# Kernel tuning notes

Measured on AMD Instinct MI355X. Metric: run time of the kernel, lower is better.

Reference implementation:

```python
import jax, jax.numpy as jnp
import numpy as np

N = 100000   # nodes
E = 1600000  # edges
IN = 3       # in_channels
H = 32       # hidden_channels
C = 10       # num_classes_dynamic (== num output classes here)
G = 64       # number of graphs in the batch


def setup_inputs() -> dict:
    key = jax.random.key(0)
    ks = jax.random.split(key, 12)
    def w(k, shape, fan_in):
        return jax.random.normal(k, shape, jnp.float32) / np.sqrt(fan_in).astype(np.float32)
    inp = {}
    inp["x"] = jax.random.normal(ks[0], (N, IN), jnp.float32)
    inp["edge_index"] = jax.random.randint(ks[1], (2, E), 0, N, jnp.int32)
    inp["batch"] = jnp.sort(jax.random.randint(ks[2], (N,), 0, G, jnp.int32))
    # per-class linear filters (DynamicEdgeConv.filters)
    inp["filt_W"] = w(ks[3], (C, IN, H), IN)
    inp["filt_b"] = jnp.zeros((C, H), jnp.float32)
    # shared edge MLP: Linear(2H,H) -> ReLU -> Linear(H,H)
    inp["mlp_W1"] = w(ks[4], (2 * H, H), 2 * H)
    inp["mlp_b1"] = jnp.zeros((H,), jnp.float32)
    inp["mlp_W2"] = w(ks[5], (H, H), H)
    inp["mlp_b2"] = jnp.zeros((H,), jnp.float32)
    # GCN layers (gcn1 input dim hardcoded 323 = IN + C*H)
    inp["gcn1_W"] = w(ks[6], (IN + C * H, H), IN + C * H)
    inp["gcn1_b"] = jnp.zeros((H,), jnp.float32)
    inp["gcn2_W"] = w(ks[7], (H, H), H)
    inp["gcn2_b"] = jnp.zeros((H,), jnp.float32)
    # classifier
    inp["cls_W"] = w(ks[8], (H, C), H)
    inp["cls_b"] = jnp.zeros((C,), jnp.float32)
    return inp


def _gcn_conv(x, W, b, row, col, dinv):
    # PyG GCNConv: add self-loops, sym-normalize, aggregate src->dst
    xw = x @ W                                   # [N, H]
    norm = dinv[row] * dinv[col]                 # [E]
    out = jax.ops.segment_sum(xw[row] * norm[:, None], col, num_segments=x.shape[0])
    out = out + xw * (dinv * dinv)[:, None]      # self-loop term, norm = 1/deg_i
    return out + b


def _forward(x, edge_index, batch, filt_W, filt_b, mlp_W1, mlp_b1, mlp_W2, mlp_b2,
             gcn1_W, gcn1_b, gcn2_W, gcn2_b, cls_W, cls_b):
    row, col = edge_index[0], edge_index[1]
    n = x.shape[0]

    # DynamicEdgeConv: per-class filter -> gather(row,col) -> edge MLP -> scatter_add into col
    def per_class(_, wb):
        Wc, bc = wb
        xc = x @ Wc + bc                                      # [N, H]
        ef = jnp.concatenate([xc[row], xc[col]], axis=1)      # [E, 2H]
        h = jax.nn.relu(ef @ mlp_W1 + mlp_b1) @ mlp_W2 + mlp_b2
        return None, jax.ops.segment_sum(h, col, num_segments=n)
    _, aggs = jax.lax.scan(per_class, None, (filt_W, filt_b))  # [C, N, H]

    feat = jnp.concatenate([x, aggs.transpose(1, 0, 2).reshape(n, -1)], axis=1)  # [N, IN + C*H]

    deg = jax.ops.segment_sum(jnp.ones(row.shape[0], x.dtype), col, num_segments=n) + 1.0
    dinv = deg ** -0.5
    h1 = jax.nn.relu(_gcn_conv(feat, gcn1_W, gcn1_b, row, col, dinv))
    h2 = jax.nn.relu(_gcn_conv(h1, gcn2_W, gcn2_b, row, col, dinv))

    counts = jax.ops.segment_sum(jnp.ones(n, x.dtype), batch, num_segments=G)
    pooled = jax.ops.segment_sum(h2, batch, num_segments=G) / jnp.maximum(counts, 1.0)[:, None]
    return pooled @ cls_W + cls_b                             # [G, C]


def reference(x, edge_index, batch, filt_W, filt_b, mlp_W1, mlp_b1, mlp_W2, mlp_b2,
              gcn1_W, gcn1_b, gcn2_W, gcn2_b, cls_W, cls_b):
    return _forward(x, edge_index, batch, filt_W, filt_b, mlp_W1, mlp_b1, mlp_W2, mlp_b2,
                    gcn1_W, gcn1_b, gcn2_W, gcn2_b, cls_W, cls_b)
```

## Files before the change

### kernel.cpp

```cpp
#include <hip/hip_runtime.h>

#define NN 100000
#define NE 1600000
#define HH 32
#define CC 10
#define GG 64
#define NB 391
#define PBLK 100
#define ECH 16000
#define MTOT (NB * PBLK)
#define MSB ((MTOT + 255) / 256)

typedef _Float16 half8 __attribute__((ext_vector_type(8)));
typedef _Float16 half2v __attribute__((ext_vector_type(2)));
typedef float f32x4 __attribute__((ext_vector_type(4)));

__device__ __forceinline__ half2v bch(int v) { return __builtin_bit_cast(half2v, v); }


__global__ void precompute_small(const float* __restrict__ fW, const float* __restrict__ fb,
                                 const float* __restrict__ W1, const float* __restrict__ b1,
                                 const float* __restrict__ W2, const float* __restrict__ b2,
                                 const float* __restrict__ g1W, float* __restrict__ tab,
                                 _Float16* __restrict__ Mfrag) {
    int c = blockIdx.x;
    int k = threadIdx.x >> 5;
    int j = threadIdx.x & 31;
    float m = 0.f;
    for (int mm = 0; mm < 32; ++mm)
        m += W2[k * 32 + mm] * g1W[(3 + 32 * c + mm) * 32 + j];
    tab[2240 + c * 1024 + k * 32 + j] = m;

    if (k < 3) {
        float a = 0.f, b = 0.f;
        for (int i = 0; i < 32; ++i) {
            float w = fW[c * 96 + k * 32 + i];
            a += w * W1[i * 32 + j];
            b += w * W1[(32 + i) * 32 + j];
        }
        tab[c * 96 + k * 32 + j] = a;
        tab[960 + c * 96 + k * 32 + j] = b;
    } else if (k == 3) {
        float h = b1[j];
        for (int i = 0; i < 32; ++i)
            h += fb[c * 32 + i] * (W1[i * 32 + j] + W1[(32 + i) * 32 + j]);
        tab[1920 + c * 32 + j] = h;
    } else if (k == 4 && c == 0) {
        float t = 0.f;
        for (int cc2 = 0; cc2 < CC; ++cc2)
            for (int mm = 0; mm < 32; ++mm)
                t += b2[mm] * g1W[(3 + 32 * cc2 + mm) * 32 + j];
        tab[12480 + j] = t;
    }
    __syncthreads();
    {
        int jch = k;
        int jcol = j;
        float v = tab[2240 + c * 1024 + jch * 32 + jcol];
        int knew = (c >> 1) * 64 + 2 * jch + (c & 1);
        int kc = knew >> 5, within = knew & 31;
        int jt = jcol >> 4;
        int lq = within >> 3, ii = within & 7;
        int lidx = lq * 16 + (jcol & 15);
        int flat = ((kc * 2 + jt) * 64 + lidx) * 8 + ii;
        Mfrag[flat] = (_Float16)v;
    }
}

__global__ void bucket_hist(const int* __restrict__ ei, int* __restrict__ mat) {
    __shared__ int h[NB];
    int blk = blockIdx.x, tid = threadIdx.x;
    for (int i = tid; i < NB; i += 256) h[i] = 0;
    __syncthreads();
    int base = blk * ECH;
    for (int k = tid; k < ECH; k += 256)
        atomicAdd(&h[ei[NE + base + k] >> 8], 1);
    __syncthreads();
    for (int i = tid; i < NB; i += 256) mat[i * PBLK + blk] = h[i];
}

__global__ void scan_m1(const int* __restrict__ mat, int* __restrict__ msum) {
    __shared__ int sh[256];
    int b = blockIdx.x, t = threadIdx.x;
    int i = b * 256 + t;
    sh[t] = (i < MTOT) ? mat[i] : 0;
    __syncthreads();
    for (int off = 128; off > 0; off >>= 1) {
        if (t < off) sh[t] += sh[t + off];
        __syncthreads();
    }
    if (t == 0) msum[b] = sh[0];
}

__global__ void scan_m2(int* __restrict__ msum, float* __restrict__ pooled) {
    for (int i = threadIdx.x; i < GG * 33; i += 256) pooled[i] = 0.0f;
    __shared__ int sh[256];
    int t = threadIdx.x;
    int v = (t < MSB) ? msum[t] : 0;
    sh[t] = v;
    __syncthreads();
    for (int off = 1; off < 256; off <<= 1) {
        int add = (t >= off) ? sh[t - off] : 0;
        __syncthreads();
        sh[t] += add;
        __syncthreads();
    }
    if (t < MSB) msum[t] = sh[t] - v;
}

__global__ void scan_m3(int* __restrict__ mat, const int* __restrict__ msum) {
    __shared__ int sh[256];
    int b = blockIdx.x, t = threadIdx.x;
    int i = b * 256 + t;
    int v = (i < MTOT) ? mat[i] : 0;
    sh[t] = v;
    __syncthreads();
    for (int off = 1; off < 256; off <<= 1) {
        int add = (t >= off) ? sh[t - off] : 0;
        __syncthreads();
        sh[t] += add;
        __syncthreads();
    }
    if (i < MTOT) mat[i] = sh[t] - v + msum[b];
}

__global__ void bucket_scatter(const int* __restrict__ ei, const int* __restrict__ mat,
                               unsigned int* __restrict__ part) {
    __shared__ int bas[NB];
    __shared__ int cur[NB];
    int blk = blockIdx.x, tid = threadIdx.x;
    for (int i = tid; i < NB; i += 256) { bas[i] = mat[i * PBLK + blk]; cur[i] = 0; }
    __syncthreads();
    int base = blk * ECH;
    for (int k = tid; k < ECH; k += 256) {
        int e = base + k;
        int r = ei[e];
        int c = ei[NE + e];
        int b = c >> 8;
        int local = atomicAdd(&cur[b], 1);
        part[bas[b] + local] = (unsigned)r | ((unsigned)(c & 255) << 24);
    }
}

__global__ void bucket_build(const unsigned int* __restrict__ part, const int* __restrict__ mat,
                             const float* __restrict__ x, int* __restrict__ csr_row,
                             int* __restrict__ ideg, int* __restrict__ offs,
                             float* __restrict__ dinv, float4* __restrict__ xpad,
                             uint4* __restrict__ xs) {
    __shared__ int lh[256];
    __shared__ int lex[256];
    __shared__ int cur[256];
    int b = blockIdx.x, tid = threadIdx.x;
    int ebase = mat[b * PBLK];
    int eend = (b == NB - 1) ? NE : mat[(b + 1) * PBLK];
    int m = eend - ebase;
    lh[tid] = 0;
    __syncthreads();
    for (int k = tid; k < m; k += 256) {
        unsigned v = part[ebase + k];
        atomicAdd(&lh[v >> 24], 1);
    }
    __syncthreads();
    int cnt = lh[tid];
    lex[tid] = cnt;
    __syncthreads();
    for (int off = 1; off < 256; off <<= 1) {
        int v = (tid >= off) ? lex[tid - off] : 0;
        __syncthreads();
        lex[tid] += v;
        __syncthreads();
    }
    int excl = lex[tid] - cnt;
    lex[tid] = excl;
    cur[tid] = 0;
    int n = b * 256 + tid;
    if (n < NN) {
        ideg[n] = cnt;
        offs[n] = ebase + excl;
        float di = rsqrtf((float)cnt + 1.0f);
        dinv[n] = di;
        float x0 = x[n * 3], x1 = x[n * 3 + 1], x2 = x[n * 3 + 2];
        xpad[n] = make_float4(x0, x1, x2, di);
        _Float16 hx = (_Float16)x0, hy = (_Float16)x1, hz = (_Float16)x2;
        half2v sx = {hx, hx}, sy = {hy, hy}, sz = {hz, hz};
        xs[n] = make_uint4(__builtin_bit_cast(unsigned int, sx),
                           __builtin_bit_cast(unsigned int, sy),
                           __builtin_bit_cast(unsigned int, sz), 0u);
    }
    if (b == 0 && tid == 0) offs[NN] = NE;
    __syncthreads();
    for (int k = tid; k < m; k += 256) {
        unsigned v = part[ebase + k];
        int cl = (int)(v >> 24);
        int r = (int)(v & 0x00FFFFFFu);
        int local = atomicAdd(&cur[cl], 1);
        csr_row[ebase + lex[cl] + local] = r;
    }
}

#define EC_PAIR(QQ, SRC) do { \
    half2v px_ = bch(__shfl((int)(QQ).x, (SRC), 64)); \
    half2v py_ = bch(__shfl((int)(QQ).y, (SRC), 64)); \
    half2v pz_ = bch(__shfl((int)(QQ).z, (SRC), 64)); \
    _Pragma("unroll") \
    for (int p = 0; p < 5; ++p) { \
        half2v v = va[p] + px_ * A0[p] + py_ * A1[p] + pz_ * A2[p]; \
        v = __builtin_elementwise_max(v, zero); \
        acc[p] += v; \
    } } while (0)

#define EC_FLUSH() do { \
    _Pragma("unroll") \
    for (int p = 0; p < 5; ++p) { \
        accf[2 * p]     += (float)acc[p].x; \
        accf[2 * p + 1] += (float)acc[p].y; \
        acc[p] = zero; \
    } } while (0)

#define EC_CHUNK_FROM(T0, QQ, C2) do { \
    int tfull_ = (C2) >> 1; \
    int t_ = (T0); \
    for (; t_ + 4 <= tfull_; t_ += 4) { \
        _Pragma("unroll") \
        for (int u = 0; u < 4; ++u) EC_PAIR(QQ, 2 * (t_ + u) + half); \
        EC_FLUSH(); \
    } \
    for (; t_ < tfull_; ++t_) EC_PAIR(QQ, 2 * t_ + half); \
    if ((C2) & 1) { \
        int src_ = (C2) - 1; \
        half2v px_ = bch(__shfl((int)(QQ).x, src_, 64)); \
        half2v py_ = bch(__shfl((int)(QQ).y, src_, 64)); \
        half2v pz_ = bch(__shfl((int)(QQ).z, src_, 64)); \
        if (half == 0) { \
            _Pragma("unroll") \
            for (int p = 0; p < 5; ++p) { \
                half2v v = va[p] + px_ * A0[p] + py_ * A1[p] + pz_ * A2[p]; \
                v = __builtin_elementwise_max(v, zero); \
                acc[p] += v; \
            } \
        } \
    } \
    EC_FLUSH(); } while (0)

__global__ __launch_bounds__(256, 4) void edgeconv_fused(
    const uint4* __restrict__ xs, const int* __restrict__ offs,
    const int* __restrict__ csr_row, const float* __restrict__ tab,
    _Float16* __restrict__ aggh) {
    int lane = threadIdx.x & 63;
    int j = lane & 31;
    int half = lane >> 5;

    half2v A0[5], A1[5], A2[5], B0[5], B1[5], B2[5], hb[5];
#pragma unroll
    for (int p = 0; p < 5; ++p) {
        int c0 = 2 * p, c1 = 2 * p + 1;
        A0[p] = half2v{(_Float16)tab[c0 * 96 + j],        (_Float16)tab[c1 * 96 + j]};
        A1[p] = half2v{(_Float16)tab[c0 * 96 + 32 + j],   (_Float16)tab[c1 * 96 + 32 + j]};
        A2[p] = half2v{(_Float16)tab[c0 * 96 + 64 + j],   (_Float16)tab[c1 * 96 + 64 + j]};
        B0[p] = half2v{(_Float16)tab[960 + c0 * 96 + j],      (_Float16)tab[960 + c1 * 96 + j]};
        B1[p] = half2v{(_Float16)tab[960 + c0 * 96 + 32 + j], (_Float16)tab[960 + c1 * 96 + 32 + j]};
        B2[p] = half2v{(_Float16)tab[960 + c0 * 96 + 64 + j], (_Float16)tab[960 + c1 * 96 + 64 + j]};
        hb[p] = half2v{(_Float16)tab[1920 + c0 * 32 + j], (_Float16)tab[1920 + c1 * 32 + j]};
    }
    const half2v zero = half2v{(_Float16)0.f, (_Float16)0.f};

    int wid = blockIdx.x * 4 + (threadIdx.x >> 6);
    const int ws = gridDim.x * 4;

    int n = wid;
    if (n >= NN) return;
    int e0 = offs[n];
    int e1 = offs[n + 1];
    uint4 qn = xs[n];
    int n2 = n + ws;
    int e0n = 0, e1n = 0;
    if (n2 < NN) { e0n = offs[n2]; e1n = offs[n2 + 1]; }
    uint4 q;
    {
        int ee = e0 + lane;
        int r0 = (ee < e1) ? csr_row[ee] : 0;
        q = xs[r0];
    }

    while (true) {
        int n3 = n2 + ws;
        int e0n2 = 0, e1n2 = 0;
        if (n3 < NN) { e0n2 = offs[n3]; e1n2 = offs[n3 + 1]; }
        uint4 qn2 = make_uint4(0u, 0u, 0u, 0u);
        if (n2 < NN) qn2 = xs[n2];

        bool multi = (e1 - e0) > 64;
        int pb = multi ? (e0 + 64) : e0n;
        int pe = multi ? e1 : e1n;
        int ee2 = pb + lane;
        int rn = (ee2 < pe) ? csr_row[ee2] : 0;

        half2v pxn = bch((int)qn.x), pyn = bch((int)qn.y), pzn = bch((int)qn.z);
        half2v va[5], acc[5];
        float accf[10];
#pragma unroll
        for (int p = 0; p < 5; ++p) {
            va[p] = hb[p] + pxn * B0[p] + pyn * B1[p] + pzn * B2[p];
            acc[p] = zero;
            accf[2 * p] = 0.f;
            accf[2 * p + 1] = 0.f;
        }

        int c2 = e1 - e0;
        if (c2 > 64) c2 = 64;
        int t0 = 0;
        if ((c2 >> 1) >= 4) {
#pragma unroll
            for (int u = 0; u < 4; ++u) EC_PAIR(q, 2 * u + half);
            EC_FLUSH();
            t0 = 4;
        }
        uint4 qpre = xs[rn];
        EC_CHUNK_FROM(t0, q, c2);

        if (multi) {
            int base = e0 + 64;
            uint4 qc = qpre;
            while (true) {
                int cc = e1 - base;
                if (cc > 64) cc = 64;
                int nb = base + 64;
                bool m2 = nb < e1;
                int pb2 = m2 ? nb : e0n;
                int pe2 = m2 ? e1 : e1n;
                int ee3 = pb2 + lane;
                int rn2 = (ee3 < pe2) ? csr_row[ee3] : 0;
                uint4 qp2 = xs[rn2];
                EC_CHUNK_FROM(0, qc, cc);
                qc = qp2;
                if (!m2) break;
                base = nb;
            }
            qpre = qc;
        }

#pragma unroll
        for (int c = 0; c < 10; ++c) accf[c] += __shfl_xor(accf[c], 32, 64);
        unsigned* arow32 = (unsigned*)(aggh + (size_t)n * 320);
        half2v d0 = {(_Float16)accf[2 * half],     (_Float16)accf[2 * half + 1]};
        half2v d1 = {(_Float16)accf[4 + 2 * half], (_Float16)accf[4 + 2 * half + 1]};
        arow32[lane]      = __builtin_bit_cast(unsigned, d0);
        arow32[64 + lane] = __builtin_bit_cast(unsigned, d1);
        if (half == 0) {
            half2v d2 = {(_Float16)accf[8], (_Float16)accf[9]};
            arow32[128 + lane] = __builtin_bit_cast(unsigned, d2);
        }

        if (n2 >= NN) return;
        n = n2;
        n2 = n3;
        e0 = e0n; e1 = e1n;
        e0n = e0n2; e1n = e1n2;
        qn = qn2;
        q = qpre;
    }
}

__global__ __launch_bounds__(256) void fold_mfma(
    const _Float16* __restrict__ aggh, const _Float16* __restrict__ MfragG,
    const float4* __restrict__ xpad, const int* __restrict__ ideg,
    const float* __restrict__ tab, const float* __restrict__ g1W,
    _Float16* __restrict__ y1) {
    __shared__ _Float16 Mf[10240];
    {
        const uint4* src = (const uint4*)MfragG;
        uint4* dst = (uint4*)Mf;
        for (int i = threadIdx.x; i < 1280; i += 256) dst[i] = src[i];
    }
    __syncthreads();

    int wave = blockIdx.x * 4 + (threadIdx.x >> 6);
    int lane = threadIdx.x & 63;
    int n0 = wave * 16;
    if (n0 >= NN) return;

    int m = lane & 15, q = lane >> 4;
    int arow_n = n0 + m;
    bool rowok = arow_n < NN;
    const _Float16* arow = aggh + (size_t)arow_n * 320 + q * 8;

    const half8* mf = (const half8*)Mf;
    f32x4 acc0 = {0.f, 0.f, 0.f, 0.f};
    f32x4 acc1 = {0.f, 0.f, 0.f, 0.f};

    for (int kc = 0; kc < 10; ++kc) {
        half8 a;
        if (rowok) a = *(const half8*)(arow + kc * 32);
        else {
#pragma unroll
            for (int i = 0; i < 8; ++i) a[i] = (_Float16)0.f;
        }
        half8 b0 = mf[(kc * 2 + 0) * 64 + lane];
        half8 b1 = mf[(kc * 2 + 1) * 64 + lane];
        acc0 = __builtin_amdgcn_mfma_f32_16x16x32_f16(a, b0, acc0, 0, 0, 0);
        acc1 = __builtin_amdgcn_mfma_f32_16x16x32_f16(a, b1, acc1, 0, 0, 0);
    }

    int jcol = lane & 15;
    float t0 = tab[12480 + jcol],      t1 = tab[12480 + 16 + jcol];
    float w00 = g1W[jcol],      w01 = g1W[32 + jcol],      w02 = g1W[64 + jcol];
    float w10 = g1W[16 + jcol], w11 = g1W[48 + jcol],      w12 = g1W[80 + jcol];
#pragma unroll
    for (int r = 0; r < 4; ++r) {
        int node = n0 + q * 4 + r;
        if (node < NN) {
            float4 xn = xpad[node];
            float dg = (float)ideg[node];
            float v0 = dg * t0 + xn.x * w00 + xn.y * w01 + xn.z * w02 + acc0[r];
            float v1 = dg * t1 + xn.x * w10 + xn.y * w11 + xn.z * w12 + acc1[r];
            y1[node * 32 + jcol]      = (_Float16)(v0 * xn.w);
            y1[node * 32 + 16 + jcol] = (_Float16)(v1 * xn.w);
        }
    }
}

__global__ __launch_bounds__(256, 8) void prop1_fused(
    const int* __restrict__ offs, const int* __restrict__ csr_row,
    const unsigned int* __restrict__ y1p, const float* __restrict__ dinv,
    const float* __restrict__ g1b, const float* __restrict__ g2W,
    unsigned int* __restrict__ y2p) {
    __shared__ float g2s[1024];
    for (int i = threadIdx.x; i < 1024; i += 256) g2s[i] = g2W[i];
    __syncthreads();

    int lane = threadIdx.x & 63;
    int l = lane & 15;
    int wid = blockIdx.x * 4 + (threadIdx.x >> 6);
    int n = wid * 4 + (lane >> 4);
    if (n >= NN) return;

    int e0 = offs[n], e1 = offs[n + 1];
    float sAl = 0.f, sAh = 0.f, sBl = 0.f, sBh = 0.f;
    int e = e0;
    if (e + 7 < e1) {
        int r[8];
#pragma unroll
        for (int u = 0; u < 8; ++u) r[u] = csr_row[e + u];
        while (true) {
            half2v p[8];
#pragma unroll
            for (int u = 0; u < 8; ++u) p[u] = __builtin_bit_cast(half2v, y1p[r[u] * 16 + l]);
            int e2 = e + 8;
            bool more = (e2 + 7 < e1);
            if (more) {
#pragma unroll
                for (int u = 0; u < 8; ++u) r[u] = csr_row[e2 + u];
            }
#pragma unroll
            for (int u = 0; u < 8; u += 2) {
                sAl += (float)p[u].x;     sAh += (float)p[u].y;
                sBl += (float)p[u + 1].x; sBh += (float)p[u + 1].y;
            }
            e = e2;
            if (!more) break;
        }
    }
    if (e + 3 < e1) {
        int r[4];
#pragma unroll
        for (int u = 0; u < 4; ++u) r[u] = csr_row[e + u];
        half2v p[4];
#pragma unroll
        for (int u = 0; u < 4; ++u) p[u] = __builtin_bit_cast(half2v, y1p[r[u] * 16 + l]);
        sAl += (float)p[0].x + (float)p[2].x; sAh += (float)p[0].y + (float)p[2].y;
        sBl += (float)p[1].x + (float)p[3].x; sBh += (float)p[1].y + (float)p[3].y;
        e += 4;
    }
    if (e + 1 < e1) {
        int r0 = csr_row[e], r1 = csr_row[e + 1];
        half2v p0 = __builtin_bit_cast(half2v, y1p[r0 * 16 + l]);
        half2v p1 = __builtin_bit_cast(half2v, y1p[r1 * 16 + l]);
        sAl += (float)p0.x; sAh += (float)p0.y;
        sBl += (float)p1.x; sBh += (float)p1.y;
        e += 2;
    }
    if (e < e1) {
        int r = csr_row[e];
        half2v p = __builtin_bit_cast(half2v, y1p[r * 16 + l]);
        sAl += (float)p.x; sAh += (float)p.y;
    }
    float di = dinv[n];
    half2v pn = __builtin_bit_cast(half2v, y1p[n * 16 + l]);
    float h1l = di * (sAl + sBl + (float)pn.x);
    float h1h = di * (sAh + sBh + (float)pn.y);
    float hl = fmaxf(h1l + g1b[2 * l], 0.f);
    float hh = fmaxf(h1h + g1b[2 * l + 1], 0.f);

    float al = 0.f, ah = 0.f;
    int base = lane & 48;
#pragma unroll
    for (int m = 0; m < 16; ++m) {
        float xl = __shfl(hl, base + m, 64);
        float xh2 = __shfl(hh, base + m, 64);
        al += xl * g2s[(2 * m) * 32 + 2 * l] + xh2 * g2s[(2 * m + 1) * 32 + 2 * l];
        ah += xl * g2s[(2 * m) * 32 + 2 * l + 1] + xh2 * g2s[(2 * m + 1) * 32 + 2 * l + 1];
    }
    half2v o = {(_Float16)(al * di), (_Float16)(ah * di)};
    y2p[n * 16 + l] = __builtin_bit_cast(unsigned int, o);
}

__global__ __launch_bounds__(256, 8) void prop2_plain(
    const int* __restrict__ offs, const int* __restrict__ csr_row,
    const unsigned int* __restrict__ y2p, const float* __restrict__ dinv,
    unsigned int* __restrict__ outp) {
    int lane = threadIdx.x & 63;
    int l = lane & 15;
    int wid = blockIdx.x * 4 + (threadIdx.x >> 6);
    int n = wid * 4 + (lane >> 4);
    if (n >= NN) return;

    int e0 = offs[n], e1 = offs[n + 1];
    float sAl = 0.f, sAh = 0.f, sBl = 0.f, sBh = 0.f;
    int e = e0;
    if (e + 7 < e1) {
        int r[8];
#pragma unroll
        for (int u = 0; u < 8; ++u) r[u] = csr_row[e + u];
        while (true) {
            half2v p[8];
#pragma unroll
            for (int u = 0; u < 8; ++u) p[u] = __builtin_bit_cast(half2v, y2p[r[u] * 16 + l]);
            int e2 = e + 8;
            bool more = (e2 + 7 < e1);
            if (more) {
#pragma unroll
                for (int u = 0; u < 8; ++u) r[u] = csr_row[e2 + u];
            }
#pragma unroll
            for (int u = 0; u < 8; u += 2) {
                sAl += (float)p[u].x;     sAh += (float)p[u].y;
                sBl += (float)p[u + 1].x; sBh += (float)p[u + 1].y;
            }
            e = e2;
            if (!more) break;
        }
    }
    if (e + 3 < e1) {
        int r[4];
#pragma unroll
        for (int u = 0; u < 4; ++u) r[u] = csr_row[e + u];
        half2v p[4];
#pragma unroll
        for (int u = 0; u < 4; ++u) p[u] = __builtin_bit_cast(half2v, y2p[r[u] * 16 + l]);
        sAl += (float)p[0].x + (float)p[2].x; sAh += (float)p[0].y + (float)p[2].y;
        sBl += (float)p[1].x + (float)p[3].x; sBh += (float)p[1].y + (float)p[3].y;
        e += 4;
    }
    if (e + 1 < e1) {
        int r0 = csr_row[e], r1 = csr_row[e + 1];
        half2v p0 = __builtin_bit_cast(half2v, y2p[r0 * 16 + l]);
        half2v p1 = __builtin_bit_cast(half2v, y2p[r1 * 16 + l]);
        sAl += (float)p0.x; sAh += (float)p0.y;
        sBl += (float)p1.x; sBh += (float)p1.y;
        e += 2;
    }
    if (e < e1) {
        int r = csr_row[e];
        half2v p = __builtin_bit_cast(half2v, y2p[r * 16 + l]);
        sAl += (float)p.x; sAh += (float)p.y;
    }
    float di = dinv[n];
    half2v pn = __builtin_bit_cast(half2v, y2p[n * 16 + l]);
    half2v o = {(_Float16)(di * (sAl + sBl + (float)pn.x)),
                (_Float16)(di * (sAh + sBh + (float)pn.y))};
    outp[n * 16 + l] = __builtin_bit_cast(unsigned int, o);
}

__global__ void pool_seg(const _Float16* __restrict__ h2, const float* __restrict__ g2b,
                         const int* __restrict__ batch, float* __restrict__ pooled,
                         float* __restrict__ counts) {
    int grp = threadIdx.x >> 5, j = threadIdx.x & 31;
    int base = (blockIdx.x * 8 + grp) * 64;
    if (base >= NN) return;
    float bj = g2b[j];
    float acc = 0.f, cnt = 0.f;
    int curg = -1;
    int lim = base + 64;
    if (lim > NN) lim = NN;
    for (int n = base; n < lim; ++n) {
        int g = batch[n];
        if (g != curg) {
            if (curg >= 0) {
                atomicAdd(&pooled[curg * 32 + j], acc);
                if (j == 0) atomicAdd(&counts[curg], cnt);
            }
            curg = g; acc = 0.f; cnt = 0.f;
        }
        acc += fmaxf((float)h2[n * 32 + j] + bj, 0.f);
        cnt += 1.f;
    }
    if (curg >= 0) {
        atomicAdd(&pooled[curg * 32 + j], acc);
        if (j == 0) atomicAdd(&counts[curg], cnt);
    }
}

__global__ void final_kernel(const float* __restrict__ pooled, const float* __restrict__ counts,
                             const float* __restrict__ clsW, const float* __restrict__ clsb,
                             float* __restrict__ out) {
    int tid = threadIdx.x;
    if (tid >= GG * CC) return;
    int g = tid / CC, cc = tid % CC;
    float inv = 1.0f / fmaxf(counts[g], 1.0f);
    float s = clsb[cc];
    for (int j = 0; j < 32; ++j) s += (pooled[g * 32 + j] * inv) * clsW[j * CC + cc];
    out[g * CC + cc] = s;
}

extern "C" void kernel_launch(void* const* d_in, const int* in_sizes, int n_in,
                              void* d_out, int out_size, void* d_ws, size_t ws_size,
                              hipStream_t stream) {
    const float* x     = (const float*)d_in[0];
    const int*   ei    = (const int*)d_in[1];
    const int*   batch = (const int*)d_in[2];
    const float* fW    = (const float*)d_in[3];
    const float* fb    = (const float*)d_in[4];
    const float* W1    = (const float*)d_in[5];
    const float* b1    = (const float*)d_in[6];
    const float* W2    = (const float*)d_in[7];
    const float* b2    = (const float*)d_in[8];
    const float* g1W   = (const float*)d_in[9];
    const float* g1b   = (const float*)d_in[10];
    const float* g2W   = (const float*)d_in[11];
    const float* g2b   = (const float*)d_in[12];
    const float* clsW  = (const float*)d_in[13];
    const float* clsb  = (const float*)d_in[14];
    float* out = (float*)d_out;

    float4*         xpad    = (float4*)d_ws;
    uint4*          xs      = (uint4*)(xpad + NN);
    _Float16*       aggh    = (_Float16*)(xs + NN);
    unsigned int*   part    = (unsigned int*)aggh;
    int*            csr_row = (int*)(aggh + (size_t)NN * 320);
    int*            mat     = (int*)(csr_row + NE);
    int*            msum    = mat + MTOT;
    int*            ideg    = msum + 256;
    int*            offs    = ideg + NN;
    float*          dinv    = (float*)(offs + NN + 1);
    float*          tab     = dinv + NN;
    _Float16*       Mfrag   = (_Float16*)(tab + 16384);
    _Float16*       y1      = Mfrag + 10240;
    unsigned int*   y2p     = (unsigned int*)(y1 + (size_t)NN * 32);
    unsigned int*   h2p     = y2p + (size_t)NN * 16;
    float*          pooled  = (float*)(h2p + (size_t)NN * 16);
    float*          counts  = pooled + GG * 32;

    const int propBlocks = (NN + 15) / 16;
    const int foldBlocks = ((NN + 15) / 16 + 3) / 4;

    precompute_small<<<10, 1024, 0, stream>>>(fW, fb, W1, b1, W2, b2, g1W, tab, Mfrag);

    bucket_hist<<<PBLK, 256, 0, stream>>>(ei, mat);
    scan_m1<<<MSB, 256, 0, stream>>>(mat, msum);
    scan_m2<<<1, 256, 0, stream>>>(msum, pooled);
    scan_m3<<<MSB, 256, 0, stream>>>(mat, msum);
    bucket_scatter<<<PBLK, 256, 0, stream>>>(ei, mat, part);
    bucket_build<<<NB, 256, 0, stream>>>(part, mat, x, csr_row, ideg, offs, dinv, xpad, xs);

    edgeconv_fused<<<2048, 256, 0, stream>>>(xs, offs, csr_row, tab, aggh);
    fold_mfma<<<foldBlocks, 256, 0, stream>>>(aggh, Mfrag, xpad, ideg, tab, g1W, y1);

    prop1_fused<<<propBlocks, 256, 0, stream>>>(offs, csr_row, (const unsigned int*)y1,
                                                dinv, g1b, g2W, y2p);
    prop2_plain<<<propBlocks, 256, 0, stream>>>(offs, csr_row, y2p, dinv, h2p);
    pool_seg<<<(NN + 511) / 512, 256, 0, stream>>>((const _Float16*)h2p, g2b, batch,
                                                   pooled, counts);
    final_kernel<<<1, 640, 0, stream>>>(pooled, counts, clsW, clsb, out);
}
```

Measured before the change: 362.5 us.

## Retune bucket partitioning, double-buffer prop1 gathers, split prop2 edges across slots

Changes the bucket partition count and edge chunk size used by the CSR build. In prop1, the gathered neighbor values for the next group of 8 edges are loaded before the current group is summed, so the gathers overlap the accumulation. prop2 is rewritten so one wavefront handles one node, with four 16-lane slots each taking a subset of its edges and combining them through cross-lane shuffles. This shortens the serial per-node edge loop and evens out load across lanes, at the cost of launching four times as many blocks and leaving many lanes idle on low-degree nodes.

```diff
diff --git a/kernel.cpp b/kernel.cpp
--- a/kernel.cpp
+++ b/kernel.cpp
@@ -6,8 +6,8 @@
 #define CC 10
 #define GG 64
 #define NB 391
-#define PBLK 100
-#define ECH 16000
+#define PBLK 160
+#define ECH 10000
 #define MTOT (NB * PBLK)
 #define MSB ((MTOT + 255) / 256)
 
@@ -435,29 +435,39 @@
     if (n >= NN) return;
 
     int e0 = offs[n], e1 = offs[n + 1];
+    float di = dinv[n];
+    half2v pn = __builtin_bit_cast(half2v, y1p[n * 16 + l]);
     float sAl = 0.f, sAh = 0.f, sBl = 0.f, sBh = 0.f;
     int e = e0;
     if (e + 7 < e1) {
-        int r[8];
-#pragma unroll
-        for (int u = 0; u < 8; ++u) r[u] = csr_row[e + u];
+        half2v p0[8];
+        {
+            int r0[8];
+#pragma unroll
+            for (int u = 0; u < 8; ++u) r0[u] = csr_row[e + u];
+#pragma unroll
+            for (int u = 0; u < 8; ++u) p0[u] = __builtin_bit_cast(half2v, y1p[r0[u] * 16 + l]);
+        }
         while (true) {
-            half2v p[8];
-#pragma unroll
-            for (int u = 0; u < 8; ++u) p[u] = __builtin_bit_cast(half2v, y1p[r[u] * 16 + l]);
             int e2 = e + 8;
             bool more = (e2 + 7 < e1);
+            half2v p1[8];
             if (more) {
-#pragma unroll
-                for (int u = 0; u < 8; ++u) r[u] = csr_row[e2 + u];
+                int r1[8];
+#pragma unroll
+                for (int u = 0; u < 8; ++u) r1[u] = csr_row[e2 + u];
+#pragma unroll
+                for (int u = 0; u < 8; ++u) p1[u] = __builtin_bit_cast(half2v, y1p[r1[u] * 16 + l]);
             }
 #pragma unroll
             for (int u = 0; u < 8; u += 2) {
-                sAl += (float)p[u].x;     sAh += (float)p[u].y;
-                sBl += (float)p[u + 1].x; sBh += (float)p[u + 1].y;
+                sAl += (float)p0[u].x;     sAh += (float)p0[u].y;
+                sBl += (float)p0[u + 1].x; sBh += (float)p0[u + 1].y;
             }
             e = e2;
             if (!more) break;
+#pragma unroll
+            for (int u = 0; u < 8; ++u) p0[u] = p1[u];
         }
     }
     if (e + 3 < e1) {
@@ -484,8 +494,6 @@
         half2v p = __builtin_bit_cast(half2v, y1p[r * 16 + l]);
         sAl += (float)p.x; sAh += (float)p.y;
     }
-    float di = dinv[n];
-    half2v pn = __builtin_bit_cast(half2v, y1p[n * 16 + l]);
     float h1l = di * (sAl + sBl + (float)pn.x);
     float h1h = di * (sAh + sBh + (float)pn.y);
     float hl = fmaxf(h1l + g1b[2 * l], 0.f);
@@ -504,71 +512,53 @@
     y2p[n * 16 + l] = __builtin_bit_cast(unsigned int, o);
 }
 
-__global__ __launch_bounds__(256, 8) void prop2_plain(
+__global__ __launch_bounds__(256, 8) void prop2_slot(
     const int* __restrict__ offs, const int* __restrict__ csr_row,
     const unsigned int* __restrict__ y2p, const float* __restrict__ dinv,
     unsigned int* __restrict__ outp) {
     int lane = threadIdx.x & 63;
     int l = lane & 15;
-    int wid = blockIdx.x * 4 + (threadIdx.x >> 6);
-    int n = wid * 4 + (lane >> 4);
+    int slot = lane >> 4;
+    int n = blockIdx.x * 4 + (threadIdx.x >> 6);
     if (n >= NN) return;
 
     int e0 = offs[n], e1 = offs[n + 1];
-    float sAl = 0.f, sAh = 0.f, sBl = 0.f, sBh = 0.f;
-    int e = e0;
-    if (e + 7 < e1) {
-        int r[8];
-#pragma unroll
-        for (int u = 0; u < 8; ++u) r[u] = csr_row[e + u];
-        while (true) {
-            half2v p[8];
-#pragma unroll
-            for (int u = 0; u < 8; ++u) p[u] = __builtin_bit_cast(half2v, y2p[r[u] * 16 + l]);
-            int e2 = e + 8;
-            bool more = (e2 + 7 < e1);
-            if (more) {
-#pragma unroll
-                for (int u = 0; u < 8; ++u) r[u] = csr_row[e2 + u];
-            }
-#pragma unroll
-            for (int u = 0; u < 8; u += 2) {
-                sAl += (float)p[u].x;     sAh += (float)p[u].y;
-                sBl += (float)p[u + 1].x; sBh += (float)p[u + 1].y;
-            }
-            e = e2;
-            if (!more) break;
-        }
-    }
-    if (e + 3 < e1) {
-        int r[4];
-#pragma unroll
-        for (int u = 0; u < 4; ++u) r[u] = csr_row[e + u];
-        half2v p[4];
-#pragma unroll
-        for (int u = 0; u < 4; ++u) p[u] = __builtin_bit_cast(half2v, y2p[r[u] * 16 + l]);
-        sAl += (float)p[0].x + (float)p[2].x; sAh += (float)p[0].y + (float)p[2].y;
-        sBl += (float)p[1].x + (float)p[3].x; sBh += (float)p[1].y + (float)p[3].y;
-        e += 4;
-    }
-    if (e + 1 < e1) {
-        int r0 = csr_row[e], r1 = csr_row[e + 1];
-        half2v p0 = __builtin_bit_cast(half2v, y2p[r0 * 16 + l]);
-        half2v p1 = __builtin_bit_cast(half2v, y2p[r1 * 16 + l]);
-        sAl += (float)p0.x; sAh += (float)p0.y;
-        sBl += (float)p1.x; sBh += (float)p1.y;
-        e += 2;
-    }
-    if (e < e1) {
-        int r = csr_row[e];
-        half2v p = __builtin_bit_cast(half2v, y2p[r * 16 + l]);
-        sAl += (float)p.x; sAh += (float)p.y;
-    }
     float di = dinv[n];
     half2v pn = __builtin_bit_cast(half2v, y2p[n * 16 + l]);
-    half2v o = {(_Float16)(di * (sAl + sBl + (float)pn.x)),
-                (_Float16)(di * (sAh + sBh + (float)pn.y))};
-    outp[n * 16 + l] = __builtin_bit_cast(unsigned int, o);
+    float sl = 0.f, sh = 0.f;
+    int e = e0;
+    if (e < e1) {
+        int i0 = e + slot, i1 = e + 4 + slot;
+        int rA = csr_row[(i0 < e1) ? i0 : (e1 - 1)];
+        int rB = csr_row[(i1 < e1) ? i1 : (e1 - 1)];
+        bool okA = i0 < e1, okB = i1 < e1;
+        while (true) {
+            half2v pA = __builtin_bit_cast(half2v, y2p[rA * 16 + l]);
+            half2v pB = __builtin_bit_cast(half2v, y2p[rB * 16 + l]);
+            int en = e + 8;
+            bool more = en < e1;
+            int rA2 = 0, rB2 = 0;
+            bool okA2 = false, okB2 = false;
+            if (more) {
+                int j0 = en + slot, j1 = en + 4 + slot;
+                rA2 = csr_row[(j0 < e1) ? j0 : (e1 - 1)];
+                rB2 = csr_row[(j1 < e1) ? j1 : (e1 - 1)];
+                okA2 = j0 < e1; okB2 = j1 < e1;
+            }
+            if (okA) { sl += (float)pA.x; sh += (float)pA.y; }
+            if (okB) { sl += (float)pB.x; sh += (float)pB.y; }
+            e = en;
+            if (!more) break;
+            rA = rA2; rB = rB2; okA = okA2; okB = okB2;
+        }
+    }
+    sl += __shfl_xor(sl, 16, 64); sl += __shfl_xor(sl, 32, 64);
+    sh += __shfl_xor(sh, 16, 64); sh += __shfl_xor(sh, 32, 64);
+    if (slot == 0) {
+        half2v o = {(_Float16)(di * (sl + (float)pn.x)),
+                    (_Float16)(di * (sh + (float)pn.y))};
+        outp[n * 16 + l] = __builtin_bit_cast(unsigned int, o);
+    }
 }
 
 __global__ void pool_seg(const _Float16* __restrict__ h2, const float* __restrict__ g2b,
@@ -652,6 +642,7 @@
 
     const int propBlocks = (NN + 15) / 16;
     const int foldBlocks = ((NN + 15) / 16 + 3) / 4;
+    const int slotBlocks = (NN + 3) / 4;
 
     precompute_small<<<10, 1024, 0, stream>>>(fW, fb, W1, b1, W2, b2, g1W, tab, Mfrag);
 
@@ -667,7 +658,7 @@
 
     prop1_fused<<<propBlocks, 256, 0, stream>>>(offs, csr_row, (const unsigned int*)y1,
                                                 dinv, g1b, g2W, y2p);
-    prop2_plain<<<propBlocks, 256, 0, stream>>>(offs, csr_row, y2p, dinv, h2p);
+    prop2_slot<<<slotBlocks, 256, 0, stream>>>(offs, csr_row, y2p, dinv, h2p);
     pool_seg<<<(NN + 511) / 512, 256, 0, stream>>>((const _Float16*)h2p, g2b, batch,
                                                    pooled, counts);
     final_kernel<<<1, 640, 0, stream>>>(pooled, counts, clsW, clsb, out);
```

Result: no change. 358.6 us (median of 2 runs) (-1.1%).
